# Kernel tuning notes

Measured on AMD Instinct MI355X. Metric: run time of the kernel, lower is better.

The kernel has to match this reference:

```python
import math
import jax, jax.numpy as jnp
import numpy as np

B, S, D, H = 2, 4096, 512, 8
DH = D // H


def setup_inputs() -> dict:
    key = jax.random.key(0)
    ks = jax.random.split(key, 12)
    lim = 1.0 / math.sqrt(D)
    u = lambda k, shp: jax.random.uniform(k, shp, jnp.float32, -lim, lim)
    return {
        "x": jax.random.normal(ks[0], (B, S, D), jnp.float32),
        "gamma": jax.random.uniform(ks[1], (B, S, 1), jnp.float32),
        "Wq": u(ks[2], (D, D)), "bq": u(ks[3], (D,)),
        "Wk": u(ks[4], (D, D)), "bk": u(ks[5], (D,)),
        "Wv": u(ks[6], (D, D)), "bv": u(ks[7], (D,)),
        "Wo": u(ks[8], (D, D)), "bo": u(ks[9], (D,)),
    }


def reference(x, gamma, Wq, bq, Wk, bk, Wv, bv, Wo, bo):
    b, s, d = x.shape
    # projections (torch Linear: x @ W.T + b), split heads -> [B,H,S,DH]
    def proj(W, bias):
        return (x @ W.T + bias).reshape(b, s, H, DH).transpose(0, 2, 1, 3)
    q, k, v = proj(Wq, bq), proj(Wk, bk), proj(Wv, bv)

    scores = jnp.einsum("bhsd,bhtd->bhst", q, k) / math.sqrt(DH)  # [B,H,S,S]
    causal = jnp.triu(jnp.ones((s, s), bool), k=1)  # True above diagonal
    neg_inf = jnp.float32(-jnp.inf)
    scores = jnp.where(causal[None, None], neg_inf, scores)

    # hyperbolic positional bias: -log1p(gamma_i * max(i-j, 0) + 1e-8)
    pos = jnp.arange(s)
    delta = jnp.clip(pos[:, None] - pos[None, :], 0).astype(jnp.float32)  # [S,S]
    gamma_q = gamma[:, :, 0][:, :, None]  # [B,S,1]
    hyper = -jnp.log1p(gamma_q * delta + 1e-8)  # [B,S,S]
    hyper = jnp.where(causal[None], neg_inf, hyper)
    scores = scores + hyper[:, None]  # [B,H,S,S]

    attn = jax.nn.softmax(scores, axis=-1)
    out = jnp.einsum("bhst,bhtd->bhsd", attn, v)  # [B,H,S,DH]
    out = out.transpose(0, 2, 1, 3).reshape(b, s, d)
    return out @ Wo.T + bo
```

## Files before the change

### kernel.cpp

```cpp
#include <hip/hip_runtime.h>
#include <hip/hip_bf16.h>

#define Bb 2
#define Ss 4096
#define Dd 512
#define Hh 8
#define DHh 64

typedef __attribute__((ext_vector_type(8))) short short8;
typedef __attribute__((ext_vector_type(4))) float floatx4;

static __device__ __forceinline__ ushort bfbits(float f) {
  union { __hip_bfloat16 h; ushort u; } cv;
  cv.h = __float2bfloat16(f);
  return cv.u;
}

static __device__ __forceinline__ unsigned int packhi(float a, float b) {
  union { float f; unsigned int u; } ca, cb; ca.f = a; cb.f = b;
  return (ca.u >> 16) | (cb.u & 0xffff0000u);
}

__global__ void cvt_all(const float* __restrict__ x,
                        const float* __restrict__ w0, const float* __restrict__ w1,
                        const float* __restrict__ w2, const float* __restrict__ w3,
                        ushort* __restrict__ out) {
  const int XN4 = (Bb * Ss * Dd) / 4;
  const int WN4 = (Dd * Dd) / 4;
  int i = blockIdx.x * blockDim.x + threadIdx.x;
  if (i >= XN4 + 4 * WN4) return;
  const float* s; int li;
  if (i < XN4) { s = x; li = i; }
  else {
    int t = i - XN4; int j = t >> 16; li = t & (WN4 - 1);
    s = (j == 0) ? w0 : (j == 1) ? w1 : (j == 2) ? w2 : w3;
  }
  float4 f = ((const float4*)s)[li];
  ushort4 u;
  u.x = bfbits(f.x); u.y = bfbits(f.y); u.z = bfbits(f.z); u.w = bfbits(f.w);
  ((ushort4*)out)[i] = u;
}

static __device__ __forceinline__ int vperm(int s0) {
  int kb = (s0 >> 4) & 3, gq = (s0 >> 2) & 3;
  return (s0 & ~63) | ((kb >> 1) << 5) | (gq << 3) | ((kb & 1) << 2);
}

#define LDQK(buf, k0)                                                          \
  _Pragma("unroll")                                                            \
  for (int rb = 0; rb < 4; ++rb)                                               \
    af[buf][rb] = *(const short8*)(ap + (size_t)rb * 16 * 512 + (k0));         \
  _Pragma("unroll")                                                            \
  for (int cb = 0; cb < 4; ++cb)                                               \
    bf[buf][cb] = *(const short8*)(bp + (size_t)cb * 16 * 512 + (k0));

__global__ __launch_bounds__(256) void qkv_gemm(
    const ushort* __restrict__ xb,
    const ushort* __restrict__ Wq, const ushort* __restrict__ Wk, const ushort* __restrict__ Wv,
    const float* __restrict__ bq, const float* __restrict__ bk, const float* __restrict__ bv,
    ushort* __restrict__ qo, ushort* __restrict__ ko, ushort* __restrict__ vo)
{
  int mb = blockIdx.x / 12, rest = blockIdx.x % 12;
  int which = rest >> 2, nb = rest & 3;
  const ushort* Bw  = (which == 0) ? Wq : (which == 1) ? Wk : Wv;
  const float* bias = (which == 0) ? bq : (which == 1) ? bk : bv;
  int lane = threadIdx.x & 63, w = threadIdx.x >> 6;
  int wr = w & 1, wc = w >> 1;
  int g = lane >> 4, ln = lane & 15;
  int m0 = mb * 128 + wr * 64;
  int c0 = nb * 128 + wc * 64;
  const ushort* ap = xb + (size_t)(m0 + ln) * 512 + g * 8;
  const ushort* bp = Bw + (size_t)(c0 + ln) * 512 + g * 8;
  floatx4 acc[4][4] = {};
  short8 af[2][4], bf[2][4];
  LDQK(0, 0)
#pragma unroll
  for (int it = 0; it < 16; ++it) {
    int cur = it & 1;
    if (it < 15) { LDQK(cur ^ 1, (it + 1) * 32) }
#pragma unroll
    for (int rb = 0; rb < 4; ++rb)
#pragma unroll
      for (int cb = 0; cb < 4; ++cb)
        acc[rb][cb] = __builtin_amdgcn_mfma_f32_16x16x32_bf16(af[cur][rb], bf[cur][cb], acc[rb][cb], 0, 0, 0);
  }
  float scale = (which == 0) ? 0.18033688011112042f : 1.0f;
#pragma unroll
  for (int rb = 0; rb < 4; ++rb)
#pragma unroll
    for (int cb = 0; cb < 4; ++cb) {
      int col = c0 + cb * 16 + ln;
      float bv_ = bias[col];
      int hh = col >> 6, dh = col & 63;
      if (which == 2) {
        int i0 = m0 + rb * 16 + g * 4;
        int bI = i0 >> 12, s0 = i0 & (Ss - 1);
        ushort4 pk;
        pk.x = bfbits(acc[rb][cb][0] + bv_);
        pk.y = bfbits(acc[rb][cb][1] + bv_);
        pk.z = bfbits(acc[rb][cb][2] + bv_);
        pk.w = bfbits(acc[rb][cb][3] + bv_);
        *(ushort4*)(vo + (((size_t)bI * Hh + hh) * DHh + dh) * Ss + vperm(s0)) = pk;
      } else {
        ushort* outp = (which == 0) ? qo : ko;
#pragma unroll
        for (int r = 0; r < 4; ++r) {
          int i = m0 + rb * 16 + g * 4 + r;
          int bI = i >> 12, s = i & (Ss - 1);
          outp[(((size_t)bI * Hh + hh) * Ss + s) * DHh + dh] = bfbits((acc[rb][cb][r] + bv_) * scale);
        }
      }
    }
}

#define LD32(buf, k0)                                                          \
  af[buf][0] = *(const short8*)(ap + (k0));                                    \
  af[buf][1] = *(const short8*)(ap + 16 * 512 + (k0));                         \
  _Pragma("unroll")                                                            \
  for (int ns = 0; ns < 4; ++ns)                                               \
    bfr[buf][ns] = *(const short8*)(bp + (size_t)ns * 16 * 512 + (k0));

__global__ __launch_bounds__(256) void gemm_out(
    const ushort* __restrict__ A, const ushort* __restrict__ Bw,
    const float* __restrict__ bias, float* __restrict__ outp)
{
  int mb = blockIdx.x >> 3, nb = blockIdx.x & 7;
  int lane = threadIdx.x & 63, w = threadIdx.x >> 6;
  int g = lane >> 4, ln = lane & 15;
  int m0 = mb * 128 + w * 32;
  const ushort* ap = A + (size_t)(m0 + ln) * 512 + g * 8;
  const ushort* bp = Bw + (size_t)(nb * 64 + ln) * 512 + g * 8;
  floatx4 acc[2][4] = {};
  short8 af[2][2], bfr[2][4];
  LD32(0, 0)
#pragma unroll
  for (int it = 0; it < 16; ++it) {
    int cur = it & 1;
    if (it < 15) { LD32(cur ^ 1, (it + 1) * 32) }
#pragma unroll
    for (int ns = 0; ns < 4; ++ns) {
      acc[0][ns] = __builtin_amdgcn_mfma_f32_16x16x32_bf16(af[cur][0], bfr[cur][ns], acc[0][ns], 0, 0, 0);
      acc[1][ns] = __builtin_amdgcn_mfma_f32_16x16x32_bf16(af[cur][1], bfr[cur][ns], acc[1][ns], 0, 0, 0);
    }
  }
#pragma unroll
  for (int rb = 0; rb < 2; ++rb)
#pragma unroll
    for (int ns = 0; ns < 4; ++ns) {
      int col = nb * 64 + ns * 16 + ln;
      float bv_ = bias[col];
#pragma unroll
      for (int r = 0; r < 4; ++r)
        outp[(size_t)(m0 + rb * 16 + g * 4 + r) * 512 + col] = acc[rb][ns][r] + bv_;
    }
}

__global__ __launch_bounds__(256) void flash9(
    const ushort* __restrict__ q, const ushort* __restrict__ k,
    const ushort* __restrict__ vt, const float* __restrict__ gamma,
    ushort* __restrict__ o)
{
  __shared__ __align__(16) float Pacc[2][64][34];
  __shared__ __align__(16) ushort Tb[2][16 * 72];

  int z = blockIdx.x;
  int bh = z & 15;
  int b = bh >> 3, hh = bh & 7;
  int qsel = (z >> 4) & 1;
  int p = z >> 5;
  int c = p + 1;

  int tid = threadIdx.x;
  int wv = tid >> 6, lane = tid & 63;
  int g = lane >> 4, ln = lane & 15;

  {
    float* pz = &Pacc[0][0][0];
#pragma unroll
    for (int i = 0; i < 17; ++i) pz[tid + 256 * i] = 0.0f;
  }
  __syncthreads();

  const ushort* kp = k + ((size_t)bh * Ss + ln) * DHh + g * 8;
  const ushort* vp = vt + ((size_t)bh * DHh + ln) * Ss + g * 8;

  int bw = 16 * wv + (wv > 0 ? 1 : 0);
  int ew = 16 * (wv + 1) + 1;

  for (int seg = 0; seg < 2; ++seg) {
    int lo, hi, ut;
    if (seg == 0) { lo = bw; hi = min(ew, c); ut = p; }
    else { int s = max(bw, c); lo = s - c; hi = ew - c; ut = 63 - p; }
    if (lo >= hi) continue;

    int t = 2 * ut + qsel;
    int q0 = t * 32;
    int ktm = ut;

    const ushort* qp = q + ((size_t)bh * Ss + q0 + ln) * DHh + g * 8;
    short8 qf00 = *(const short8*)qp;
    short8 qf01 = *(const short8*)(qp + 32);
    short8 qf10 = *(const short8*)(qp + 16 * DHh);
    short8 qf11 = *(const short8*)(qp + 16 * DHh + 32);

    int qrow0 = q0 + ln, qrow1 = q0 + 16 + ln;
    float gm0 = gamma[(size_t)b * Ss + qrow0];
    float gm1 = gamma[(size_t)b * Ss + qrow1];
    float l2[2] = {0.0f, 0.0f};
    floatx4 oacc[2][4] = {};

    short8 kfl[4], kfh[4], vf[8];
    int kb0 = lo * 64;
#pragma unroll
    for (int ns = 0; ns < 4; ++ns) {
      kfl[ns] = *(const short8*)(kp + (size_t)(kb0 + ns * 16) * DHh);
      kfh[ns] = *(const short8*)(kp + (size_t)(kb0 + ns * 16) * DHh + 32);
    }
#pragma unroll
    for (int cc = 0; cc < 8; ++cc)
      vf[cc] = *(const short8*)(vp + (size_t)((cc & 3) * 16) * Ss + kb0 + (cc >> 2) * 32);

    for (int kt = lo; kt < hi; ++kt) {
      int kbase = kt * 64;
      float sv[2][16];
#pragma unroll
      for (int ns = 0; ns < 4; ++ns) {
        floatx4 z0 = {}, z1 = {};
        z0 = __builtin_amdgcn_mfma_f32_16x16x32_bf16(kfl[ns], qf00, z0, 0, 0, 0);
        z0 = __builtin_amdgcn_mfma_f32_16x16x32_bf16(kfh[ns], qf01, z0, 0, 0, 0);
        z1 = __builtin_amdgcn_mfma_f32_16x16x32_bf16(kfl[ns], qf10, z1, 0, 0, 0);
        z1 = __builtin_amdgcn_mfma_f32_16x16x32_bf16(kfh[ns], qf11, z1, 0, 0, 0);
#pragma unroll
        for (int r = 0; r < 4; ++r) { sv[0][ns * 4 + r] = z0[r]; sv[1][ns * 4 + r] = z1[r]; }
      }
      if (kt + 1 < hi) {
        const ushort* kn = kp + (size_t)(kbase + 64) * DHh;
#pragma unroll
        for (int ns = 0; ns < 4; ++ns) {
          kfl[ns] = *(const short8*)(kn + (size_t)(ns * 16) * DHh);
          kfh[ns] = *(const short8*)(kn + (size_t)(ns * 16) * DHh + 32);
        }
      }
      bool last = (kt == ktm);
      short8 pfrag[2][2];
#pragma unroll
      for (int qb = 0; qb < 2; ++qb) {
        int qrow = qb ? qrow1 : qrow0;
        float gm = qb ? gm1 : gm0;
        int db = qrow - kbase - g * 4;
        float fd = (float)db;
        float rsub[4] = {0.0f, 0.0f, 0.0f, 0.0f};
        if (last) {
#pragma unroll
          for (int e = 0; e < 16; ++e) {
            int off = (e >> 2) * 16 + (e & 3);
            if (db - off < 0) sv[qb][e] = -1e30f;
            float delta = fmaxf(fd - (float)off, 0.0f);
            float wt = __builtin_amdgcn_rcpf(fmaf(gm, delta, 1.0f));
            float pv = __builtin_amdgcn_exp2f(sv[qb][e]) * wt;
            rsub[e & 3] += pv;
            sv[qb][e] = pv;
          }
        } else {
#pragma unroll
          for (int e = 0; e < 16; ++e) {
            float delta = fd - (float)((e >> 2) * 16 + (e & 3));
            float wt = __builtin_amdgcn_rcpf(fmaf(gm, delta, 1.0f));
            float pv = __builtin_amdgcn_exp2f(sv[qb][e]) * wt;
            rsub[e & 3] += pv;
            sv[qb][e] = pv;
          }
        }
        l2[qb] += (rsub[0] + rsub[1]) + (rsub[2] + rsub[3]);
#pragma unroll
        for (int cc = 0; cc < 2; ++cc) {
          uint4 pkd;
          pkd.x = packhi(sv[qb][8 * cc + 0], sv[qb][8 * cc + 1]);
          pkd.y = packhi(sv[qb][8 * cc + 2], sv[qb][8 * cc + 3]);
          pkd.z = packhi(sv[qb][8 * cc + 4], sv[qb][8 * cc + 5]);
          pkd.w = packhi(sv[qb][8 * cc + 6], sv[qb][8 * cc + 7]);
          pfrag[qb][cc] = *(short8*)&pkd;
        }
      }
#pragma unroll
      for (int cc = 0; cc < 2; ++cc)
#pragma unroll
        for (int ds = 0; ds < 4; ++ds) {
          oacc[0][ds] = __builtin_amdgcn_mfma_f32_16x16x32_bf16(vf[cc * 4 + ds], pfrag[0][cc], oacc[0][ds], 0, 0, 0);
          oacc[1][ds] = __builtin_amdgcn_mfma_f32_16x16x32_bf16(vf[cc * 4 + ds], pfrag[1][cc], oacc[1][ds], 0, 0, 0);
        }
      if (kt + 1 < hi) {
#pragma unroll
        for (int cc = 0; cc < 8; ++cc)
          vf[cc] = *(const short8*)(vp + (size_t)((cc & 3) * 16) * Ss + kbase + 64 + (cc >> 2) * 32);
      }
    }

#pragma unroll
    for (int qb = 0; qb < 2; ++qb) {
#pragma unroll
      for (int ds = 0; ds < 4; ++ds)
#pragma unroll
        for (int r = 0; r < 4; ++r)
          atomicAdd(&Pacc[seg][lane][qb * 16 + ds * 4 + r], oacc[qb][ds][r]);
      atomicAdd(&Pacc[seg][lane][32 + qb], l2[qb]);
    }
  }

  __syncthreads();
  if (wv < 2) {
    int ut = wv ? (63 - p) : p;
    int q0 = (2 * ut + qsel) * 32;
#pragma unroll
    for (int qb = 0; qb < 2; ++qb) {
      float l = Pacc[wv][lane][32 + qb];
      l += __shfl_xor(l, 16);
      l += __shfl_xor(l, 32);
      float linv = 1.0f / l;
      ushort* tb = &Tb[wv][0];
#pragma unroll
      for (int ds = 0; ds < 4; ++ds)
#pragma unroll
        for (int r = 0; r < 4; ++r)
          tb[ln * 72 + ds * 16 + g * 4 + r] = bfbits(Pacc[wv][lane][qb * 16 + ds * 4 + r] * linv);
      short8 v0 = *(const short8*)(tb + ln * 72 + g * 16);
      short8 v1 = *(const short8*)(tb + ln * 72 + g * 16 + 8);
      size_t oa = ((size_t)b * Ss + q0 + qb * 16 + ln) * Dd + hh * DHh + g * 16;
      *(short8*)(o + oa) = v0;
      *(short8*)(o + oa + 8) = v1;
    }
  }
}

extern "C" void kernel_launch(void* const* d_in, const int* in_sizes, int n_in,
                              void* d_out, int out_size, void* d_ws, size_t ws_size,
                              hipStream_t stream) {
  const float* x     = (const float*)d_in[0];
  const float* gamma = (const float*)d_in[1];
  const float* Wq    = (const float*)d_in[2];
  const float* bq    = (const float*)d_in[3];
  const float* Wk    = (const float*)d_in[4];
  const float* bk    = (const float*)d_in[5];
  const float* Wv    = (const float*)d_in[6];
  const float* bv    = (const float*)d_in[7];
  const float* Wo    = (const float*)d_in[8];
  const float* bo    = (const float*)d_in[9];

  const size_t NX = (size_t)Bb * Ss * Dd;
  const size_t NW = (size_t)Dd * Dd;
  ushort* xb  = (ushort*)d_ws;
  ushort* Wqb = xb + NX;
  ushort* Wkb = Wqb + NW;
  ushort* Wvb = Wkb + NW;
  ushort* Wob = Wvb + NW;
  ushort* qb  = Wob + NW;
  ushort* kb  = qb + NX;
  ushort* vtb = kb + NX;
  ushort* ab  = vtb + NX;

  const int total4 = (int)(NX / 4 + 4 * (NW / 4));
  cvt_all<<<(total4 + 255) / 256, 256, 0, stream>>>(x, Wq, Wk, Wv, Wo, xb);

  qkv_gemm<<<64 * 12, 256, 0, stream>>>(xb, Wqb, Wkb, Wvb, bq, bk, bv, qb, kb, vtb);

  flash9<<<1024, 256, 0, stream>>>(qb, kb, vtb, gamma, ab);

  gemm_out<<<512, 256, 0, stream>>>(ab, Wob, bo, (float*)d_out);
}
```

Baseline: 305.6 us.

## Split each query tile's key range evenly across four waves, processed phase by phase

New measurement: 338.9 us. +10.9%, slower.

```diff
diff --git a/kernel.cpp b/kernel.cpp
--- a/kernel.cpp
+++ b/kernel.cpp
@@ -155,179 +155,181 @@
     }
 }
 
-__global__ __launch_bounds__(256) void flash9(
+__global__ __launch_bounds__(256) void flash10(
     const ushort* __restrict__ q, const ushort* __restrict__ k,
     const ushort* __restrict__ vt, const float* __restrict__ gamma,
     ushort* __restrict__ o)
 {
-  __shared__ __align__(16) float Pacc[2][64][34];
-  __shared__ __align__(16) ushort Tb[2][16 * 72];
+  __shared__ __align__(16) float Pacc[64][35];
+  __shared__ __align__(16) ushort Tb[16 * 72];
 
   int z = blockIdx.x;
   int bh = z & 15;
   int b = bh >> 3, hh = bh & 7;
   int qsel = (z >> 4) & 1;
-  int p = z >> 5;
-  int c = p + 1;
+  int P = z >> 5;
 
   int tid = threadIdx.x;
   int wv = tid >> 6, lane = tid & 63;
   int g = lane >> 4, ln = lane & 15;
 
   {
-    float* pz = &Pacc[0][0][0];
-#pragma unroll
-    for (int i = 0; i < 17; ++i) pz[tid + 256 * i] = 0.0f;
+    float* pz = &Pacc[0][0];
+    for (int i = tid; i < 64 * 35; i += 256) pz[i] = 0.0f;
   }
   __syncthreads();
 
   const ushort* kp = k + ((size_t)bh * Ss + ln) * DHh + g * 8;
   const ushort* vp = vt + ((size_t)bh * DHh + ln) * Ss + g * 8;
 
-  int bw = 16 * wv + (wv > 0 ? 1 : 0);
-  int ew = 16 * (wv + 1) + 1;
-
-  for (int seg = 0; seg < 2; ++seg) {
-    int lo, hi, ut;
-    if (seg == 0) { lo = bw; hi = min(ew, c); ut = p; }
-    else { int s = max(bw, c); lo = s - c; hi = ew - c; ut = 63 - p; }
-    if (lo >= hi) continue;
-
-    int t = 2 * ut + qsel;
-    int q0 = t * 32;
-    int ktm = ut;
-
-    const ushort* qp = q + ((size_t)bh * Ss + q0 + ln) * DHh + g * 8;
-    short8 qf00 = *(const short8*)qp;
-    short8 qf01 = *(const short8*)(qp + 32);
-    short8 qf10 = *(const short8*)(qp + 16 * DHh);
-    short8 qf11 = *(const short8*)(qp + 16 * DHh + 32);
-
-    int qrow0 = q0 + ln, qrow1 = q0 + 16 + ln;
-    float gm0 = gamma[(size_t)b * Ss + qrow0];
-    float gm1 = gamma[(size_t)b * Ss + qrow1];
+  for (int phase = 0; phase < 2; ++phase) {
+    int u = phase ? (63 - P) : P;
+    int nkt = u + 1;
+    int ktm = u;
+    int qd = nkt >> 2, rr = nkt & 3;
+    int lo = wv * qd + min(wv, rr);
+    int hi = lo + qd + (wv < rr ? 1 : 0);
+    int q0 = (2 * u + qsel) * 32;
+
     float l2[2] = {0.0f, 0.0f};
     floatx4 oacc[2][4] = {};
 
-    short8 kfl[4], kfh[4], vf[8];
-    int kb0 = lo * 64;
-#pragma unroll
-    for (int ns = 0; ns < 4; ++ns) {
-      kfl[ns] = *(const short8*)(kp + (size_t)(kb0 + ns * 16) * DHh);
-      kfh[ns] = *(const short8*)(kp + (size_t)(kb0 + ns * 16) * DHh + 32);
-    }
-#pragma unroll
-    for (int cc = 0; cc < 8; ++cc)
-      vf[cc] = *(const short8*)(vp + (size_t)((cc & 3) * 16) * Ss + kb0 + (cc >> 2) * 32);
-
-    for (int kt = lo; kt < hi; ++kt) {
-      int kbase = kt * 64;
-      float sv[2][16];
+    if (lo < hi) {
+      const ushort* qp = q + ((size_t)bh * Ss + q0 + ln) * DHh + g * 8;
+      short8 qf00 = *(const short8*)qp;
+      short8 qf01 = *(const short8*)(qp + 32);
+      short8 qf10 = *(const short8*)(qp + 16 * DHh);
+      short8 qf11 = *(const short8*)(qp + 16 * DHh + 32);
+
+      int qrow0 = q0 + ln, qrow1 = q0 + 16 + ln;
+      float gm0 = gamma[(size_t)b * Ss + qrow0];
+      float gm1 = gamma[(size_t)b * Ss + qrow1];
+
+      short8 kfl[4], kfh[4], vf[8];
+      int kb0 = lo * 64;
 #pragma unroll
       for (int ns = 0; ns < 4; ++ns) {
-        floatx4 z0 = {}, z1 = {};
-        z0 = __builtin_amdgcn_mfma_f32_16x16x32_bf16(kfl[ns], qf00, z0, 0, 0, 0);
-        z0 = __builtin_amdgcn_mfma_f32_16x16x32_bf16(kfh[ns], qf01, z0, 0, 0, 0);
-        z1 = __builtin_amdgcn_mfma_f32_16x16x32_bf16(kfl[ns], qf10, z1, 0, 0, 0);
-        z1 = __builtin_amdgcn_mfma_f32_16x16x32_bf16(kfh[ns], qf11, z1, 0, 0, 0);
-#pragma unroll
-        for (int r = 0; r < 4; ++r) { sv[0][ns * 4 + r] = z0[r]; sv[1][ns * 4 + r] = z1[r]; }
+        kfl[ns] = *(const short8*)(kp + (size_t)(kb0 + ns * 16) * DHh);
+        kfh[ns] = *(const short8*)(kp + (size_t)(kb0 + ns * 16) * DHh + 32);
       }
-      if (kt + 1 < hi) {
-        const ushort* kn = kp + (size_t)(kbase + 64) * DHh;
+#pragma unroll
+      for (int cc = 0; cc < 8; ++cc)
+        vf[cc] = *(const short8*)(vp + (size_t)((cc & 3) * 16) * Ss + kb0 + (cc >> 2) * 32);
+
+      for (int kt = lo; kt < hi; ++kt) {
+        int kbase = kt * 64;
+        float sv[2][16];
 #pragma unroll
         for (int ns = 0; ns < 4; ++ns) {
-          kfl[ns] = *(const short8*)(kn + (size_t)(ns * 16) * DHh);
-          kfh[ns] = *(const short8*)(kn + (size_t)(ns * 16) * DHh + 32);
+          floatx4 z0 = {}, z1 = {};
+          z0 = __builtin_amdgcn_mfma_f32_16x16x32_bf16(kfl[ns], qf00, z0, 0, 0, 0);
+          z0 = __builtin_amdgcn_mfma_f32_16x16x32_bf16(kfh[ns], qf01, z0, 0, 0, 0);
+          z1 = __builtin_amdgcn_mfma_f32_16x16x32_bf16(kfl[ns], qf10, z1, 0, 0, 0);
+          z1 = __builtin_amdgcn_mfma_f32_16x16x32_bf16(kfh[ns], qf11, z1, 0, 0, 0);
+#pragma unroll
+          for (int r = 0; r < 4; ++r) { sv[0][ns * 4 + r] = z0[r]; sv[1][ns * 4 + r] = z1[r]; }
+        }
+        if (kt + 1 < hi) {
+          const ushort* kn = kp + (size_t)(kbase + 64) * DHh;
+#pragma unroll
+          for (int ns = 0; ns < 4; ++ns) {
+            kfl[ns] = *(const short8*)(kn + (size_t)(ns * 16) * DHh);
+            kfh[ns] = *(const short8*)(kn + (size_t)(ns * 16) * DHh + 32);
+          }
+        }
+        bool last = (kt == ktm);
+        short8 pfrag[2][2];
+#pragma unroll
+        for (int qb = 0; qb < 2; ++qb) {
+          int qrow = qb ? qrow1 : qrow0;
+          float gm = qb ? gm1 : gm0;
+          int db = qrow - kbase - g * 4;
+          float fd = (float)db;
+          float base = fmaf(gm, fd, 1.0f);
+          float rsub[4] = {0.0f, 0.0f, 0.0f, 0.0f};
+          if (last) {
+#pragma unroll
+            for (int e = 0; e < 16; ++e) {
+              int off = (e >> 2) * 16 + (e & 3);
+              if (db - off < 0) sv[qb][e] = -1e30f;
+              float delta = fmaxf(fd - (float)off, 0.0f);
+              float wt = __builtin_amdgcn_rcpf(fmaf(gm, delta, 1.0f));
+              float pv = __builtin_amdgcn_exp2f(sv[qb][e]) * wt;
+              rsub[e & 3] += pv;
+              sv[qb][e] = pv;
+            }
+          } else {
+#pragma unroll
+            for (int e = 0; e < 16; ++e) {
+              float off = (float)((e >> 2) * 16 + (e & 3));
+              float wt = __builtin_amdgcn_rcpf(fmaf(gm, -off, base));
+              float pv = __builtin_amdgcn_exp2f(sv[qb][e]) * wt;
+              rsub[e & 3] += pv;
+              sv[qb][e] = pv;
+            }
+          }
+          l2[qb] += (rsub[0] + rsub[1]) + (rsub[2] + rsub[3]);
+#pragma unroll
+          for (int cc = 0; cc < 2; ++cc) {
+            uint4 pkd;
+            pkd.x = packhi(sv[qb][8 * cc + 0], sv[qb][8 * cc + 1]);
+            pkd.y = packhi(sv[qb][8 * cc + 2], sv[qb][8 * cc + 3]);
+            pkd.z = packhi(sv[qb][8 * cc + 4], sv[qb][8 * cc + 5]);
+            pkd.w = packhi(sv[qb][8 * cc + 6], sv[qb][8 * cc + 7]);
+            pfrag[qb][cc] = *(short8*)&pkd;
+          }
+        }
+#pragma unroll
+        for (int cc = 0; cc < 2; ++cc)
+#pragma unroll
+          for (int ds = 0; ds < 4; ++ds) {
+            oacc[0][ds] = __builtin_amdgcn_mfma_f32_16x16x32_bf16(vf[cc * 4 + ds], pfrag[0][cc], oacc[0][ds], 0, 0, 0);
+            oacc[1][ds] = __builtin_amdgcn_mfma_f32_16x16x32_bf16(vf[cc * 4 + ds], pfrag[1][cc], oacc[1][ds], 0, 0, 0);
+          }
+        if (kt + 1 < hi) {
+#pragma unroll
+          for (int cc = 0; cc < 8; ++cc)
+            vf[cc] = *(const short8*)(vp + (size_t)((cc & 3) * 16) * Ss + kbase + 64 + (cc >> 2) * 32);
         }
       }
-      bool last = (kt == ktm);
-      short8 pfrag[2][2];
+    }
+
+#pragma unroll
+    for (int qb = 0; qb < 2; ++qb) {
+#pragma unroll
+      for (int ds = 0; ds < 4; ++ds)
+#pragma unroll
+        for (int r = 0; r < 4; ++r)
+          atomicAdd(&Pacc[lane][qb * 16 + ds * 4 + r], oacc[qb][ds][r]);
+      atomicAdd(&Pacc[lane][32 + qb], l2[qb]);
+    }
+    __syncthreads();
+
+    if (wv == 0) {
 #pragma unroll
       for (int qb = 0; qb < 2; ++qb) {
-        int qrow = qb ? qrow1 : qrow0;
-        float gm = qb ? gm1 : gm0;
-        int db = qrow - kbase - g * 4;
-        float fd = (float)db;
-        float rsub[4] = {0.0f, 0.0f, 0.0f, 0.0f};
-        if (last) {
-#pragma unroll
-          for (int e = 0; e < 16; ++e) {
-            int off = (e >> 2) * 16 + (e & 3);
-            if (db - off < 0) sv[qb][e] = -1e30f;
-            float delta = fmaxf(fd - (float)off, 0.0f);
-            float wt = __builtin_amdgcn_rcpf(fmaf(gm, delta, 1.0f));
-            float pv = __builtin_amdgcn_exp2f(sv[qb][e]) * wt;
-            rsub[e & 3] += pv;
-            sv[qb][e] = pv;
-          }
-        } else {
-#pragma unroll
-          for (int e = 0; e < 16; ++e) {
-            float delta = fd - (float)((e >> 2) * 16 + (e & 3));
-            float wt = __builtin_amdgcn_rcpf(fmaf(gm, delta, 1.0f));
-            float pv = __builtin_amdgcn_exp2f(sv[qb][e]) * wt;
-            rsub[e & 3] += pv;
-            sv[qb][e] = pv;
-          }
-        }
-        l2[qb] += (rsub[0] + rsub[1]) + (rsub[2] + rsub[3]);
-#pragma unroll
-        for (int cc = 0; cc < 2; ++cc) {
-          uint4 pkd;
-          pkd.x = packhi(sv[qb][8 * cc + 0], sv[qb][8 * cc + 1]);
-          pkd.y = packhi(sv[qb][8 * cc + 2], sv[qb][8 * cc + 3]);
-          pkd.z = packhi(sv[qb][8 * cc + 4], sv[qb][8 * cc + 5]);
-          pkd.w = packhi(sv[qb][8 * cc + 6], sv[qb][8 * cc + 7]);
-          pfrag[qb][cc] = *(short8*)&pkd;
-        }
+        float l = Pacc[lane][32 + qb];
+        l += __shfl_xor(l, 16);
+        l += __shfl_xor(l, 32);
+        float linv = 1.0f / l;
+        ushort* tb = &Tb[0];
+#pragma unroll
+        for (int ds = 0; ds < 4; ++ds)
+#pragma unroll
+          for (int r = 0; r < 4; ++r)
+            tb[ln * 72 + ds * 16 + g * 4 + r] = bfbits(Pacc[lane][qb * 16 + ds * 4 + r] * linv);
+        short8 v0 = *(const short8*)(tb + ln * 72 + g * 16);
+        short8 v1 = *(const short8*)(tb + ln * 72 + g * 16 + 8);
+        size_t oa = ((size_t)b * Ss + q0 + qb * 16 + ln) * Dd + hh * DHh + g * 16;
+        *(short8*)(o + oa) = v0;
+        *(short8*)(o + oa + 8) = v1;
       }
-#pragma unroll
-      for (int cc = 0; cc < 2; ++cc)
-#pragma unroll
-        for (int ds = 0; ds < 4; ++ds) {
-          oacc[0][ds] = __builtin_amdgcn_mfma_f32_16x16x32_bf16(vf[cc * 4 + ds], pfrag[0][cc], oacc[0][ds], 0, 0, 0);
-          oacc[1][ds] = __builtin_amdgcn_mfma_f32_16x16x32_bf16(vf[cc * 4 + ds], pfrag[1][cc], oacc[1][ds], 0, 0, 0);
-        }
-      if (kt + 1 < hi) {
-#pragma unroll
-        for (int cc = 0; cc < 8; ++cc)
-          vf[cc] = *(const short8*)(vp + (size_t)((cc & 3) * 16) * Ss + kbase + 64 + (cc >> 2) * 32);
-      }
-    }
-
-#pragma unroll
-    for (int qb = 0; qb < 2; ++qb) {
-#pragma unroll
-      for (int ds = 0; ds < 4; ++ds)
-#pragma unroll
-        for (int r = 0; r < 4; ++r)
-          atomicAdd(&Pacc[seg][lane][qb * 16 + ds * 4 + r], oacc[qb][ds][r]);
-      atomicAdd(&Pacc[seg][lane][32 + qb], l2[qb]);
-    }
-  }
-
-  __syncthreads();
-  if (wv < 2) {
-    int ut = wv ? (63 - p) : p;
-    int q0 = (2 * ut + qsel) * 32;
-#pragma unroll
-    for (int qb = 0; qb < 2; ++qb) {
-      float l = Pacc[wv][lane][32 + qb];
-      l += __shfl_xor(l, 16);
-      l += __shfl_xor(l, 32);
-      float linv = 1.0f / l;
-      ushort* tb = &Tb[wv][0];
-#pragma unroll
-      for (int ds = 0; ds < 4; ++ds)
-#pragma unroll
-        for (int r = 0; r < 4; ++r)
-          tb[ln * 72 + ds * 16 + g * 4 + r] = bfbits(Pacc[wv][lane][qb * 16 + ds * 4 + r] * linv);
-      short8 v0 = *(const short8*)(tb + ln * 72 + g * 16);
-      short8 v1 = *(const short8*)(tb + ln * 72 + g * 16 + 8);
-      size_t oa = ((size_t)b * Ss + q0 + qb * 16 + ln) * Dd + hh * DHh + g * 16;
-      *(short8*)(o + oa) = v0;
-      *(short8*)(o + oa + 8) = v1;
+    }
+    __syncthreads();
+    if (phase == 0) {
+      float* pz = &Pacc[0][0];
+      for (int i = tid; i < 64 * 35; i += 256) pz[i] = 0.0f;
+      __syncthreads();
     }
   }
 }
@@ -363,7 +365,7 @@
 
   qkv_gemm<<<64 * 12, 256, 0, stream>>>(xb, Wqb, Wkb, Wvb, bq, bk, bv, qb, kb, vtb);
 
-  flash9<<<1024, 256, 0, stream>>>(qb, kb, vtb, gamma, ab);
+  flash10<<<1024, 256, 0, stream>>>(qb, kb, vtb, gamma, ab);
 
   gemm_out<<<512, 256, 0, stream>>>(ab, Wob, bo, (float*)d_out);
 }
```
